# Kernel tuning notes

Hardware: AMD Instinct MI355X
Metric: run time of the kernel (lower is better)

Reference implementation:

```python
import jax, jax.numpy as jnp
import numpy as np

V_DIM = 2048
Q_DIM = 1024
B = 64
K = 36


def setup_inputs() -> dict:
    key = jax.random.key(0)
    ks = jax.random.split(key, 6)
    s1 = 1.0 / np.sqrt(2 * V_DIM + Q_DIM)
    s2 = 1.0 / np.sqrt(V_DIM)
    s3 = 1.0 / np.sqrt(Q_DIM)
    return {
        "v": jax.random.normal(ks[0], (B, K, V_DIM), dtype=jnp.float32),
        "q": jax.random.normal(ks[1], (B, Q_DIM), dtype=jnp.float32),
        "W1": jax.random.normal(ks[2], (V_DIM, 2 * V_DIM + Q_DIM), dtype=jnp.float32) * s1,
        "b1": jnp.zeros((V_DIM,), dtype=jnp.float32),
        "W2": jax.random.normal(ks[3], (V_DIM, V_DIM), dtype=jnp.float32) * s2,
        "b2": jnp.zeros((V_DIM,), dtype=jnp.float32),
        "W3": jax.random.normal(ks[4], (Q_DIM, Q_DIM), dtype=jnp.float32) * s3,
        "b3": jnp.zeros((Q_DIM,), dtype=jnp.float32),
    }


def reference(v, q, W1, b1, W2, b2, W3, b3):
    # FCNet = (weight-normed) Linear + ReLU; dropout disabled (eval / p=0).
    vd = W2.shape[0]
    # q embedding: [B, q_dim]
    q_emb = jax.nn.relu(q @ W3.T + b3)
    # Decompose linear1(concat(v_i, v_j, q_emb)) into three matmuls.
    Wa = W1[:, :vd]            # acts on v_i
    Wb = W1[:, vd:2 * vd]      # acts on v_j
    Wc = W1[:, 2 * vd:]        # acts on q_emb
    a = jnp.einsum('bkd,vd->bkv', v, Wa)          # [B, K, v_dim]
    bpart = jnp.einsum('bkd,vd->bkv', v, Wb)      # [B, K, v_dim]
    c = jnp.einsum('bq,vq->bv', q_emb, Wc) + b1   # [B, v_dim]
    # Pairwise ReLU then sum over j: [B, K_i, K_j, v_dim] -> [B, K, v_dim]
    pair = jax.nn.relu(a[:, :, None, :] + bpart[:, None, :, :] + c[:, None, None, :])
    x = jnp.sum(pair, axis=2)
    # linear2 + ReLU
    return jax.nn.relu(jnp.einsum('bkv,wv->bkw', x, W2) + b2)
```

## Files before the change

kernel.cpp:

```cpp
#include <hip/hip_runtime.h>

#define V_DIMC 2048
#define Q_DIMC 1024
#define BATCH  64
#define KC     36
#define MROWS  (BATCH * KC)
#define W1LD   (2 * V_DIMC + Q_DIMC)

typedef __bf16 bf16_t;
typedef __attribute__((ext_vector_type(8))) __bf16 bf16x8;
typedef __attribute__((ext_vector_type(4))) __bf16 bf16x4;
typedef __attribute__((ext_vector_type(4))) float f32x4;

__device__ __forceinline__ void gload16(const bf16_t* g, bf16_t* l) {
    __builtin_amdgcn_global_load_lds(
        (const __attribute__((address_space(1))) unsigned int*)(g),
        (__attribute__((address_space(3))) unsigned int*)(l), 16, 0, 0);
}

#define MFMAI(a, b, c) __builtin_amdgcn_mfma_f32_16x16x32_bf16(a, b, c, 0, 0, 0)
#define BARX() __builtin_amdgcn_s_barrier()
#define VMC(n)  asm volatile("s_waitcnt vmcnt(" #n ")" ::: "memory")

__global__ __launch_bounds__(256) void conv_all(const float* __restrict__ v,
                                                const float* __restrict__ q,
                                                const float* __restrict__ W1,
                                                const float* __restrict__ W2,
                                                const float* __restrict__ W3,
                                                bf16_t* __restrict__ Wab,
                                                bf16_t* __restrict__ W2b,
                                                bf16_t* __restrict__ vb,
                                                bf16_t* __restrict__ W3b,
                                                bf16_t* __restrict__ Wcb,
                                                bf16_t* __restrict__ qb) {
    const int t = blockIdx.x * 256 + threadIdx.x;
    const float* src;
    bf16_t* dst;
    if (t < 2097152) {
        size_t idx = (size_t)t * 4;
        int row = (int)(idx >> 11), col = (int)(idx & 2047);
        src = (row < 2048) ? W1 + (size_t)row * W1LD + col
                           : W1 + (size_t)(row - 2048) * W1LD + V_DIMC + col;
        dst = Wab + idx;
    } else if (t < 3145728) {
        size_t idx = (size_t)(t - 2097152) * 4;
        src = W2 + idx; dst = W2b + idx;
    } else if (t < 4325376) {
        size_t idx = (size_t)(t - 3145728) * 4;
        src = v + idx; dst = vb + idx;
    } else if (t < 4587520) {
        size_t idx = (size_t)(t - 4325376) * 4;
        src = W3 + idx; dst = W3b + idx;
    } else if (t < 5111808) {
        size_t idx = (size_t)(t - 4587520) * 4;
        int row = (int)(idx >> 10), col = (int)(idx & 1023);
        src = W1 + (size_t)row * W1LD + 2 * V_DIMC + col;
        dst = Wcb + idx;
    } else {
        size_t idx = (size_t)(t - 5111808) * 4;
        src = q + idx; dst = qb + idx;
    }
    float4 f = *reinterpret_cast<const float4*>(src);
    bf16x4 o;
    o[0] = (bf16_t)f.x; o[1] = (bf16_t)f.y; o[2] = (bf16_t)f.z; o[3] = (bf16_t)f.w;
    *reinterpret_cast<bf16x4*>(dst) = o;
}

template <int MODE>
__global__ __launch_bounds__(512) void qgemm(const bf16_t* __restrict__ A,
                                             const bf16_t* __restrict__ B,
                                             void* __restrict__ out,
                                             const float* __restrict__ bias) {
    constexpr int K = 1024;
    constexpr int NDIM = (MODE == 0) ? Q_DIMC : V_DIMC;
    __shared__ float red[8][4096];
    const int tid = threadIdx.x;
    const int w = tid >> 6, l = tid & 63;
    const int n0 = blockIdx.x * 64;
    const int fr = l & 15, lq = l >> 4;
    const bf16_t* Ab = A + (size_t)(w * 128) + lq * 8;
    const bf16_t* Bb = B + (size_t)n0 * K + (size_t)(w * 128) + lq * 8;

    f32x4 acc[4][4] = {};
#pragma unroll
    for (int ks = 0; ks < 4; ++ks) {
        bf16x8 aF[4], bF[4];
#pragma unroll
        for (int mi = 0; mi < 4; ++mi)
            aF[mi] = *(const bf16x8*)(Ab + (size_t)(mi * 16 + fr) * K + ks * 32);
#pragma unroll
        for (int ni = 0; ni < 4; ++ni)
            bF[ni] = *(const bf16x8*)(Bb + (size_t)(ni * 16 + fr) * K + ks * 32);
#pragma unroll
        for (int mi = 0; mi < 4; ++mi)
#pragma unroll
            for (int ni = 0; ni < 4; ++ni)
                acc[mi][ni] = MFMAI(aF[mi], bF[ni], acc[mi][ni]);
    }

    const int rb = lq * 4;
#pragma unroll
    for (int mi = 0; mi < 4; ++mi)
#pragma unroll
        for (int ni = 0; ni < 4; ++ni)
#pragma unroll
            for (int j = 0; j < 4; ++j)
                red[w][(mi * 16 + rb + j) * 64 + ni * 16 + fr] = acc[mi][ni][j];
    __syncthreads();

    const int row = tid >> 3, cb = (tid & 7) * 8;
    float s[8] = {};
#pragma unroll
    for (int ww = 0; ww < 8; ++ww) {
        f32x4 v0 = *(const f32x4*)&red[ww][row * 64 + cb];
        f32x4 v1 = *(const f32x4*)&red[ww][row * 64 + cb + 4];
#pragma unroll
        for (int j = 0; j < 4; ++j) { s[j] += v0[j]; s[4 + j] += v1[j]; }
    }
    if (MODE == 0) {
        bf16x8 o;
#pragma unroll
        for (int j = 0; j < 8; ++j)
            o[j] = (bf16_t)fmaxf(s[j] + bias[n0 + cb + j], 0.f);
        *reinterpret_cast<bf16x8*>((bf16_t*)out + (size_t)row * NDIM + n0 + cb) = o;
    } else {
        float4 r0, r1;
        float* rr[2] = {&r0.x, &r1.x};
#pragma unroll
        for (int h = 0; h < 2; ++h)
#pragma unroll
            for (int j = 0; j < 4; ++j)
                rr[h][j] = s[h * 4 + j] + bias[n0 + cb + h * 4 + j];
        float* op = (float*)out + (size_t)row * NDIM + n0 + cb;
        *reinterpret_cast<float4*>(op) = r0;
        *reinterpret_cast<float4*>(op + 4) = r1;
    }
}

template <int MODE, int MF>
__global__ __launch_bounds__(512) void gemm8p(const bf16_t* __restrict__ A,
                                              const bf16_t* __restrict__ Bm,
                                              bf16_t* __restrict__ out0,
                                              bf16_t* __restrict__ out1,
                                              bf16_t* __restrict__ out2) {
    constexpr int K = 2048;
    constexpr int MH = MF / 2;
    const int z = (MODE == 2) ? (int)blockIdx.z : 0;
    const int NT = (MODE == 2) ? ((z == 2) ? 10 : 11) : 32;
    const int kb = (MODE == 2) ? z * 704 : 0;
    __shared__ bf16_t ldsA[2][MF * 2048];
    __shared__ bf16_t ldsB[2][2][8192];
    const int tid = threadIdx.x;
    const int w = tid >> 6, l = tid & 63;
    const int wm = w >> 2, wn = w & 3;

    int bx, by;
    if (MODE == 0) {
        const int flat = (int)blockIdx.y * 16 + (int)blockIdx.x;
        const int xcd = flat & 7, idx = flat >> 3;
        bx = (xcd & 3) * 4 + (idx & 3);
        by = (xcd >> 2) * 6 + (idx >> 2);
    } else {
        bx = (int)blockIdx.x; by = (int)blockIdx.y;
    }
    const int m0 = by * (MF * 32);
    const int n0 = bx * 256;
    const size_t sK = (size_t)K;

    const int arow = tid >> 3;
    const bf16_t* gA = A + (size_t)(m0 + arow) * sK + kb
                         + (size_t)(((tid & 7) ^ (arow & 7)) << 3);
    const int brow = tid >> 2;
    const bf16_t* gB = Bm + (size_t)(n0 + brow) * sK + kb
                          + (size_t)(((tid & 3) ^ ((tid >> 3) & 3)) << 3);
    const int stW = w * 512;

    auto STGA = [&](int T) {
#pragma unroll
        for (int p = 0; p < MH; ++p)
            gload16(gA + (size_t)(p * 64) * sK + (size_t)T * 64,
                    &ldsA[T & 1][p * 4096 + stW]);
    };
    auto STGB = [&](int ks, int T) {
        const bf16_t* g_ = gB + (size_t)T * 64 + ks * 32;
        gload16(g_, &ldsB[T & 1][ks][stW]);
        gload16(g_ + (size_t)128 * sK, &ldsB[T & 1][ks][4096 + stW]);
    };

    const int fr = l & 15, lq = l >> 4;
    const int sw0 = (lq ^ (fr & 7)) << 4;
    const int sw1 = ((4 | lq) ^ (fr & 7)) << 4;
    const int bsw = (lq ^ ((fr >> 1) & 3)) << 4;
    const int aro = fr * 128;
    const int bro = (wn * 64 + fr) * 64 + bsw;

    f32x4 acc[MF][4] = {};

    STGA(0);
    STGB(0, 0);
    STGB(1, 0);
    VMC(0);
    BARX();

    for (int T = 0; T < NT; ++T) {
        const char* pa  = (const char*)&ldsA[T & 1][0] + wm * (MF * 2048);
        const char* pb0 = (const char*)&ldsB[T & 1][0][0];
        const char* pb1 = (const char*)&ldsB[T & 1][1][0];
        bf16x8 aF[MF], bF[4];

#pragma unroll
        for (int mi = 0; mi < MF; ++mi)
            aF[mi] = *(const bf16x8*)(pa + mi * 2048 + aro + sw0);
#pragma unroll
        for (int ni = 0; ni < 4; ++ni)
            bF[ni] = *(const bf16x8*)(pb0 + bro + ni * 1024);
        if (T + 1 < NT) {
            STGA(T + 1);
            STGB(0, T + 1);
            STGB(1, T + 1);
        }
        BARX();
        __builtin_amdgcn_s_setprio(1);
#pragma unroll
        for (int mi = 0; mi < MF; ++mi)
#pragma unroll
            for (int ni = 0; ni < 4; ++ni)
                acc[mi][ni] = MFMAI(aF[mi], bF[ni], acc[mi][ni]);
        __builtin_amdgcn_s_setprio(0);
        BARX();

#pragma unroll
        for (int mi = 0; mi < MF; ++mi)
            aF[mi] = *(const bf16x8*)(pa + mi * 2048 + aro + sw1);
#pragma unroll
        for (int ni = 0; ni < 4; ++ni)
            bF[ni] = *(const bf16x8*)(pb1 + bro + ni * 1024);
        BARX();
        __builtin_amdgcn_s_setprio(1);
#pragma unroll
        for (int mi = 0; mi < MF; ++mi)
#pragma unroll
            for (int ni = 0; ni < 4; ++ni)
                acc[mi][ni] = MFMAI(aF[mi], bF[ni], acc[mi][ni]);
        __builtin_amdgcn_s_setprio(0);
        VMC(0);
        BARX();
    }

    bf16_t* o;
    int gn0;
    if (MODE == 0) {
        if (n0 < V_DIMC) { o = out0; gn0 = n0; }
        else             { o = out1; gn0 = n0 - V_DIMC; }
    } else {
        o = (z == 0) ? out0 : (z == 1) ? out1 : out2;
        gn0 = n0;
    }
    const int rb = lq * 4;
#pragma unroll
    for (int mi = 0; mi < MF; ++mi)
#pragma unroll
        for (int ni = 0; ni < 4; ++ni) {
            const size_t gm = (size_t)(m0 + wm * (MF * 16) + mi * 16 + rb);
            const int gn = gn0 + wn * 64 + ni * 16 + fr;
#pragma unroll
            for (int r = 0; r < 4; ++r)
                o[(gm + r) * V_DIMC + gn] = (bf16_t)acc[mi][ni][r];
        }
}

__global__ __launch_bounds__(256) void reduce_out(const bf16_t* __restrict__ p0,
                                                  const bf16_t* __restrict__ p1,
                                                  const bf16_t* __restrict__ p2,
                                                  const float* __restrict__ b2,
                                                  float* __restrict__ out) {
    const size_t t = (size_t)blockIdx.x * 256 + threadIdx.x;
    const size_t idx = t * 8;
    bf16x8 a = *reinterpret_cast<const bf16x8*>(p0 + idx);
    bf16x8 b = *reinterpret_cast<const bf16x8*>(p1 + idx);
    bf16x8 c = *reinterpret_cast<const bf16x8*>(p2 + idx);
    const int col = (int)(idx & (V_DIMC - 1));
    float4 r0, r1;
    float* rr[2] = {&r0.x, &r1.x};
#pragma unroll
    for (int h = 0; h < 2; ++h)
#pragma unroll
        for (int j = 0; j < 4; ++j)
            rr[h][j] = fmaxf((float)a[h * 4 + j] + (float)b[h * 4 + j] +
                             (float)c[h * 4 + j] + b2[col + h * 4 + j], 0.f);
    *reinterpret_cast<float4*>(out + idx) = r0;
    *reinterpret_cast<float4*>(out + idx + 4) = r1;
}

__global__ __launch_bounds__(256) void pair_kernel(const bf16_t* __restrict__ A,
                                                   const bf16_t* __restrict__ Bp,
                                                   const float* __restrict__ cbuf,
                                                   bf16_t* __restrict__ X) {
    const int v = blockIdx.x * 256 + threadIdx.x;
    const int b = blockIdx.y;
    const float cc = cbuf[b * V_DIMC + v];
    const bf16_t* Ab = A + (size_t)b * KC * V_DIMC + v;
    const bf16_t* Bb = Bp + (size_t)b * KC * V_DIMC + v;
    float av[KC], bv[KC];
#pragma unroll
    for (int k = 0; k < KC; ++k) {
        av[k] = (float)Ab[(size_t)k * V_DIMC] + cc;
        bv[k] = (float)Bb[(size_t)k * V_DIMC];
    }
    bf16_t* Xb = X + (size_t)b * KC * V_DIMC + v;
#pragma unroll
    for (int k = 0; k < KC; ++k) {
        float s = 0.f;
#pragma unroll
        for (int j = 0; j < KC; ++j) s += fmaxf(av[k] + bv[j], 0.f);
        Xb[(size_t)k * V_DIMC] = (bf16_t)s;
    }
}

extern "C" void kernel_launch(void* const* d_in, const int* in_sizes, int n_in,
                              void* d_out, int out_size, void* d_ws, size_t ws_size,
                              hipStream_t stream) {
    const float* v  = (const float*)d_in[0];
    const float* q  = (const float*)d_in[1];
    const float* W1 = (const float*)d_in[2];
    const float* b1 = (const float*)d_in[3];
    const float* W2 = (const float*)d_in[4];
    const float* b2 = (const float*)d_in[5];
    const float* W3 = (const float*)d_in[6];
    const float* b3 = (const float*)d_in[7];
    float* out = (float*)d_out;

    char* wsb = (char*)d_ws;
    bf16_t* Wab_b = (bf16_t*)wsb;
    bf16_t* W2b   = (bf16_t*)(wsb + 16777216ull);
    bf16_t* vb    = (bf16_t*)(wsb + 25165824ull);
    bf16_t* Abf   = (bf16_t*)(wsb + 34603008ull);
    bf16_t* W3b   = (bf16_t*)(wsb + 34603008ull);
    bf16_t* Wcb   = (bf16_t*)(wsb + 34603008ull + 2097152);
    bf16_t* qb    = (bf16_t*)(wsb + 34603008ull + 6291456);
    bf16_t* Bbf   = (bf16_t*)(wsb + 44040192ull);
    bf16_t* qemb  = (bf16_t*)(wsb + 53477376ull);
    float*  cbuf  = (float*) (wsb + 53608448ull);
    bf16_t* Xb    = Wab_b;

    conv_all<<<dim3(20032), 256, 0, stream>>>(v, q, W1, W2, W3, Wab_b, W2b, vb, W3b, Wcb, qb);
    qgemm<0><<<dim3(Q_DIMC / 64), 512, 0, stream>>>(qb, W3b, qemb, b3);
    qgemm<1><<<dim3(V_DIMC / 64), 512, 0, stream>>>(qemb, Wcb, cbuf, b1);

    gemm8p<0, 6><<<dim3(4096 / 256, MROWS / 192), 512, 0, stream>>>(vb, Wab_b, Abf, Bbf, nullptr);
    pair_kernel<<<dim3(V_DIMC / 256, BATCH), 256, 0, stream>>>(Abf, Bbf, cbuf, Xb);
    gemm8p<2, 8><<<dim3(V_DIMC / 256, MROWS / 256, 3), 512, 0, stream>>>(Xb, W2b, Abf, Bbf, vb);
    reduce_out<<<dim3((MROWS * V_DIMC / 8) / 256), 256, 0, stream>>>(Abf, Bbf, vb, b2, out);
}
```

Baseline: 144.2 us.

## Load GEMM B fragments directly from global into registers, bypassing LDS

Measured after the change: 165.0 us. 1.14x slower.

```diff
diff --git a/kernel.cpp b/kernel.cpp
--- a/kernel.cpp
+++ b/kernel.cpp
@@ -21,6 +21,7 @@
 #define MFMAI(a, b, c) __builtin_amdgcn_mfma_f32_16x16x32_bf16(a, b, c, 0, 0, 0)
 #define BARX() __builtin_amdgcn_s_barrier()
 #define VMC(n)  asm volatile("s_waitcnt vmcnt(" #n ")" ::: "memory")
+#define SCHEDB() __builtin_amdgcn_sched_barrier(0)
 
 __global__ __launch_bounds__(256) void conv_all(const float* __restrict__ v,
                                                 const float* __restrict__ q,
@@ -138,7 +139,7 @@
 }
 
 template <int MODE, int MF>
-__global__ __launch_bounds__(512) void gemm8p(const bf16_t* __restrict__ A,
+__global__ __launch_bounds__(512) void gemmbd(const bf16_t* __restrict__ A,
                                               const bf16_t* __restrict__ Bm,
                                               bf16_t* __restrict__ out0,
                                               bf16_t* __restrict__ out1,
@@ -149,7 +150,6 @@
     const int NT = (MODE == 2) ? ((z == 2) ? 10 : 11) : 32;
     const int kb = (MODE == 2) ? z * 704 : 0;
     __shared__ bf16_t ldsA[2][MF * 2048];
-    __shared__ bf16_t ldsB[2][2][8192];
     const int tid = threadIdx.x;
     const int w = tid >> 6, l = tid & 63;
     const int wm = w >> 2, wn = w & 3;
@@ -158,8 +158,8 @@
     if (MODE == 0) {
         const int flat = (int)blockIdx.y * 16 + (int)blockIdx.x;
         const int xcd = flat & 7, idx = flat >> 3;
-        bx = (xcd & 3) * 4 + (idx & 3);
-        by = (xcd >> 2) * 6 + (idx >> 2);
+        bx = xcd * 2 + (idx & 1);
+        by = idx >> 1;
     } else {
         bx = (int)blockIdx.x; by = (int)blockIdx.y;
     }
@@ -170,9 +170,6 @@
     const int arow = tid >> 3;
     const bf16_t* gA = A + (size_t)(m0 + arow) * sK + kb
                          + (size_t)(((tid & 7) ^ (arow & 7)) << 3);
-    const int brow = tid >> 2;
-    const bf16_t* gB = Bm + (size_t)(n0 + brow) * sK + kb
-                          + (size_t)(((tid & 3) ^ ((tid >> 3) & 3)) << 3);
     const int stW = w * 512;
 
     auto STGA = [&](int T) {
@@ -181,69 +178,72 @@
             gload16(gA + (size_t)(p * 64) * sK + (size_t)T * 64,
                     &ldsA[T & 1][p * 4096 + stW]);
     };
-    auto STGB = [&](int ks, int T) {
-        const bf16_t* g_ = gB + (size_t)T * 64 + ks * 32;
-        gload16(g_, &ldsB[T & 1][ks][stW]);
-        gload16(g_ + (size_t)128 * sK, &ldsB[T & 1][ks][4096 + stW]);
-    };
 
     const int fr = l & 15, lq = l >> 4;
     const int sw0 = (lq ^ (fr & 7)) << 4;
     const int sw1 = ((4 | lq) ^ (fr & 7)) << 4;
-    const int bsw = (lq ^ ((fr >> 1) & 3)) << 4;
     const int aro = fr * 128;
-    const int bro = (wn * 64 + fr) * 64 + bsw;
-
+
+    const bf16_t* gBp[4];
+#pragma unroll
+    for (int ni = 0; ni < 4; ++ni)
+        gBp[ni] = Bm + (size_t)(n0 + wn * 64 + ni * 16 + fr) * sK + kb + lq * 8;
+
+    bf16x8 bFa0, bFa1, bFa2, bFa3;
+    bf16x8 bFb0, bFb1, bFb2, bFb3;
     f32x4 acc[MF][4] = {};
 
     STGA(0);
-    STGB(0, 0);
-    STGB(1, 0);
-    VMC(0);
+    SCHEDB();
+    bFa0 = *(const bf16x8*)(gBp[0]); bFa1 = *(const bf16x8*)(gBp[1]);
+    bFa2 = *(const bf16x8*)(gBp[2]); bFa3 = *(const bf16x8*)(gBp[3]);
+    VMC(4);
     BARX();
 
     for (int T = 0; T < NT; ++T) {
-        const char* pa  = (const char*)&ldsA[T & 1][0] + wm * (MF * 2048);
-        const char* pb0 = (const char*)&ldsB[T & 1][0][0];
-        const char* pb1 = (const char*)&ldsB[T & 1][1][0];
-        bf16x8 aF[MF], bF[4];
-
+        const char* pa = (const char*)&ldsA[T & 1][0] + wm * (MF * 2048);
+        bf16x8 aF[MF];
+        const size_t tb = (size_t)T * 64;
+
+        bFb0 = *(const bf16x8*)(gBp[0] + tb + 32);
+        bFb1 = *(const bf16x8*)(gBp[1] + tb + 32);
+        bFb2 = *(const bf16x8*)(gBp[2] + tb + 32);
+        bFb3 = *(const bf16x8*)(gBp[3] + tb + 32);
 #pragma unroll
         for (int mi = 0; mi < MF; ++mi)
             aF[mi] = *(const bf16x8*)(pa + mi * 2048 + aro + sw0);
-#pragma unroll
-        for (int ni = 0; ni < 4; ++ni)
-            bF[ni] = *(const bf16x8*)(pb0 + bro + ni * 1024);
+        if (T + 1 < NT) STGA(T + 1);
+        SCHEDB();
+        __builtin_amdgcn_s_setprio(1);
+#pragma unroll
+        for (int mi = 0; mi < MF; ++mi) {
+            acc[mi][0] = MFMAI(aF[mi], bFa0, acc[mi][0]);
+            acc[mi][1] = MFMAI(aF[mi], bFa1, acc[mi][1]);
+            acc[mi][2] = MFMAI(aF[mi], bFa2, acc[mi][2]);
+            acc[mi][3] = MFMAI(aF[mi], bFa3, acc[mi][3]);
+        }
+        __builtin_amdgcn_s_setprio(0);
+
         if (T + 1 < NT) {
-            STGA(T + 1);
-            STGB(0, T + 1);
-            STGB(1, T + 1);
+            const size_t nb = (size_t)(T + 1) * 64;
+            bFa0 = *(const bf16x8*)(gBp[0] + nb);
+            bFa1 = *(const bf16x8*)(gBp[1] + nb);
+            bFa2 = *(const bf16x8*)(gBp[2] + nb);
+            bFa3 = *(const bf16x8*)(gBp[3] + nb);
         }
-        BARX();
-        __builtin_amdgcn_s_setprio(1);
-#pragma unroll
-        for (int mi = 0; mi < MF; ++mi)
-#pragma unroll
-            for (int ni = 0; ni < 4; ++ni)
-                acc[mi][ni] = MFMAI(aF[mi], bF[ni], acc[mi][ni]);
-        __builtin_amdgcn_s_setprio(0);
-        BARX();
-
 #pragma unroll
         for (int mi = 0; mi < MF; ++mi)
             aF[mi] = *(const bf16x8*)(pa + mi * 2048 + aro + sw1);
-#pragma unroll
-        for (int ni = 0; ni < 4; ++ni)
-            bF[ni] = *(const bf16x8*)(pb1 + bro + ni * 1024);
-        BARX();
         __builtin_amdgcn_s_setprio(1);
 #pragma unroll
-        for (int mi = 0; mi < MF; ++mi)
-#pragma unroll
-            for (int ni = 0; ni < 4; ++ni)
-                acc[mi][ni] = MFMAI(aF[mi], bF[ni], acc[mi][ni]);
+        for (int mi = 0; mi < MF; ++mi) {
+            acc[mi][0] = MFMAI(aF[mi], bFb0, acc[mi][0]);
+            acc[mi][1] = MFMAI(aF[mi], bFb1, acc[mi][1]);
+            acc[mi][2] = MFMAI(aF[mi], bFb2, acc[mi][2]);
+            acc[mi][3] = MFMAI(aF[mi], bFb3, acc[mi][3]);
+        }
         __builtin_amdgcn_s_setprio(0);
-        VMC(0);
+        if (T + 1 < NT) { VMC(4); }
         BARX();
     }
 
@@ -347,8 +347,8 @@
     qgemm<0><<<dim3(Q_DIMC / 64), 512, 0, stream>>>(qb, W3b, qemb, b3);
     qgemm<1><<<dim3(V_DIMC / 64), 512, 0, stream>>>(qemb, Wcb, cbuf, b1);
 
-    gemm8p<0, 6><<<dim3(4096 / 256, MROWS / 192), 512, 0, stream>>>(vb, Wab_b, Abf, Bbf, nullptr);
+    gemmbd<0, 6><<<dim3(4096 / 256, MROWS / 192), 512, 0, stream>>>(vb, Wab_b, Abf, Bbf, nullptr);
     pair_kernel<<<dim3(V_DIMC / 256, BATCH), 256, 0, stream>>>(Abf, Bbf, cbuf, Xb);
-    gemm8p<2, 8><<<dim3(V_DIMC / 256, MROWS / 256, 3), 512, 0, stream>>>(Xb, W2b, Abf, Bbf, vb);
+    gemmbd<2, 8><<<dim3(V_DIMC / 256, MROWS / 256, 3), 512, 0, stream>>>(Xb, W2b, Abf, Bbf, vb);
     reduce_out<<<dim3((MROWS * V_DIMC / 8) / 256), 256, 0, stream>>>(Abf, Bbf, vb, b2, out);
 }
```
